# Kernel tuning notes

Measured on AMD Instinct MI355X. Metric: run time of the kernel, lower is better.

The kernel has to match this reference:

```python
import jax, jax.numpy as jnp
import numpy as np
from jax import lax

B, L, D, H = 2, 4096, 1024, 16
K = 4            # short conv kernel size
HD = D // H      # head dim = 64
EPS = 1e-5


def causal_dw_conv(x, w):
    # depthwise causal conv: x [B,L,D], w [D,K]
    xp = jnp.pad(x, ((0, 0), (K - 1, 0), (0, 0)))
    out = xp[:, 0:L, :] * w[:, 0]
    for j in range(1, K):
        out = out + xp[:, j:j + L, :] * w[:, j]
    return out


def setup_inputs() -> dict:
    key = jax.random.key(0)
    ks = jax.random.split(key, 10)
    s = 0.02
    return {
        "hidden_states": jax.random.normal(ks[0], (B, L, D), jnp.float32),
        "Wq": jax.random.normal(ks[1], (D, D), jnp.float32) * s,
        "Wk": jax.random.normal(ks[2], (D, D), jnp.float32) * s,
        "Wv": jax.random.normal(ks[3], (D, D), jnp.float32) * s,
        "Wb": jax.random.normal(ks[4], (D, H), jnp.float32) * s,
        "conv_q": jax.random.normal(ks[5], (D, K), jnp.float32) * s,
        "conv_k": jax.random.normal(ks[6], (D, K), jnp.float32) * s,
        "conv_v": jax.random.normal(ks[7], (D, K), jnp.float32) * s,
        "o_norm_w": jnp.ones((HD,), jnp.float32),
        "Wo": jax.random.normal(ks[8], (D, D), jnp.float32) * s,
    }


def reference(hidden_states, Wq, Wk, Wv, Wb, conv_q, conv_k, conv_v, o_norm_w, Wo):
    x = hidden_states
    # projections + short causal conv with SiLU (qk_activation == 'silu')
    q = jax.nn.silu(causal_dw_conv(x @ Wq, conv_q))
    k = jax.nn.silu(causal_dw_conv(x @ Wk, conv_k))
    v = jax.nn.silu(causal_dw_conv(x @ Wv, conv_v))

    # [B,L,D] -> [L,B,H,hd] for the time scan
    def to_heads(t):
        return t.reshape(B, L, H, HD).transpose(1, 0, 2, 3)

    q, k, v = to_heads(q), to_heads(k), to_heads(v)

    # l2 qk-norm
    q = q / jnp.linalg.norm(q, axis=-1, keepdims=True)
    k = k / jnp.linalg.norm(k, axis=-1, keepdims=True)

    # beta gate [L,B,H]
    beta = jax.nn.sigmoid(x @ Wb).transpose(1, 0, 2)

    def step(S, inp):
        qt, kt, vt, bt = inp  # [B,H,hd] x3, [B,H]
        v_old = jnp.einsum('bhk,bhkv->bhv', kt, S)
        delta = (vt - v_old) * bt[..., None]
        S = S + jnp.einsum('bhk,bhv->bhkv', kt, delta)
        ot = jnp.einsum('bhk,bhkv->bhv', qt, S)
        return S, ot

    S0 = jnp.zeros((B, H, HD, HD), x.dtype)
    _, o = lax.scan(step, S0, (q, k, v, beta))  # o: [L,B,H,hd]
    o = o.transpose(1, 0, 2, 3)  # [B,L,H,hd]

    # per-head RMSNorm
    rms = jax.lax.rsqrt(jnp.mean(o * o, axis=-1, keepdims=True) + EPS)
    o = o * rms * o_norm_w

    return o.reshape(B, L, D) @ Wo
```

## Files before the change

kernel.cpp:

```cpp
#include <hip/hip_runtime.h>
#include <hip/hip_bf16.h>
#include <math.h>

#define BB 2
#define LL 4096
#define DD 1024
#define HH 16
#define HDIM 64
#define CC 64
#define NC 64
#define BH 32
#define GG 8
#define GS 8

typedef __attribute__((ext_vector_type(8))) short short8;
typedef __attribute__((ext_vector_type(4))) float f32x4;
typedef unsigned short u16;

__device__ __forceinline__ u16 f2bf(float f) {
    unsigned int u = __float_as_uint(f);
    unsigned int r = (u + 0x7fffu + ((u >> 16) & 1u)) >> 16;
    return (u16)r;
}
__device__ __forceinline__ float bf2f(u16 h) {
    return __uint_as_float((unsigned)h << 16);
}
__device__ __forceinline__ void split2(float x, u16& h, u16& l) {
    h = f2bf(x);
    l = f2bf(x - bf2f(h));
}
__device__ __forceinline__ float4 ld_bf4(const u16* p) {
    uint2 v = *(const uint2*)p;
    return make_float4(bf2f((u16)v.x), bf2f((u16)(v.x >> 16)),
                       bf2f((u16)v.y), bf2f((u16)(v.y >> 16)));
}

__device__ __forceinline__ void gld_lds16(const void* g, void* l) {
    __builtin_amdgcn_global_load_lds(
        (const __attribute__((address_space(1))) void*)g,
        (__attribute__((address_space(3))) void*)l, 16, 0, 0);
}

__device__ __forceinline__ int swz(int r, int c) {
    return (r << 6) + ((((c >> 2) ^ (r >> 2)) & 15) << 2) + (c & 3);
}
__device__ __forceinline__ int swze(int r, int c) {
    return (r << 6) + (c ^ (((r ^ (r >> 3)) & 7) << 3));
}

__device__ __forceinline__ void mm64(const u16* __restrict__ Ah, const u16* __restrict__ Al,
                                     const u16* __restrict__ Bh, const u16* __restrict__ Bl,
                                     f32x4* acc, int w, int lane) {
    const int ln = lane & 15, kg = (lane >> 4) * 8;
#pragma unroll
    for (int kb = 0; kb < 2; ++kb) {
        const int k0 = kb * 32 + kg;
        short8 ah = *(const short8*)&Ah[swze(w * 16 + ln, k0)];
        short8 al = *(const short8*)&Al[swze(w * 16 + ln, k0)];
#pragma unroll
        for (int j = 0; j < 4; ++j) {
            short8 bh = *(const short8*)&Bh[swze(j * 16 + ln, k0)];
            short8 bl = *(const short8*)&Bl[swze(j * 16 + ln, k0)];
            acc[j] = __builtin_amdgcn_mfma_f32_16x16x32_bf16(ah, bh, acc[j], 0, 0, 0);
            acc[j] = __builtin_amdgcn_mfma_f32_16x16x32_bf16(ah, bl, acc[j], 0, 0, 0);
            acc[j] = __builtin_amdgcn_mfma_f32_16x16x32_bf16(al, bh, acc[j], 0, 0, 0);
        }
    }
}
__device__ __forceinline__ void mm64_bb(const u16* __restrict__ Ah,
                                        const u16* __restrict__ Bh,
                                        f32x4* acc, int w, int lane) {
    const int ln = lane & 15, kg = (lane >> 4) * 8;
#pragma unroll
    for (int kb = 0; kb < 2; ++kb) {
        const int k0 = kb * 32 + kg;
        short8 ah = *(const short8*)&Ah[swze(w * 16 + ln, k0)];
#pragma unroll
        for (int j = 0; j < 4; ++j) {
            short8 bh = *(const short8*)&Bh[swze(j * 16 + ln, k0)];
            acc[j] = __builtin_amdgcn_mfma_f32_16x16x32_bf16(ah, bh, acc[j], 0, 0, 0);
        }
    }
}
__device__ __forceinline__ void mm64_ab(const u16* __restrict__ Ah,
                                        const u16* __restrict__ Bh, const u16* __restrict__ Bl,
                                        f32x4* acc, int w, int lane) {
    const int ln = lane & 15, kg = (lane >> 4) * 8;
#pragma unroll
    for (int kb = 0; kb < 2; ++kb) {
        const int k0 = kb * 32 + kg;
        short8 ah = *(const short8*)&Ah[swze(w * 16 + ln, k0)];
#pragma unroll
        for (int j = 0; j < 4; ++j) {
            short8 bh = *(const short8*)&Bh[swze(j * 16 + ln, k0)];
            short8 bl = *(const short8*)&Bl[swze(j * 16 + ln, k0)];
            acc[j] = __builtin_amdgcn_mfma_f32_16x16x32_bf16(ah, bh, acc[j], 0, 0, 0);
            acc[j] = __builtin_amdgcn_mfma_f32_16x16x32_bf16(ah, bl, acc[j], 0, 0, 0);
        }
    }
}

__device__ __forceinline__ void g_to_ls(const float* __restrict__ G, u16* Ah, u16* Al, int tid) {
#pragma unroll
    for (int p = 0; p < 4; ++p) {
        int flat = p * 1024 + tid * 4;
        int r = flat >> 6, c = flat & 63;
        float4 v = *(const float4*)&G[flat];
        u16 h0, l0, h1, l1, h2, l2, h3, l3;
        split2(v.x, h0, l0); split2(v.y, h1, l1);
        split2(v.z, h2, l2); split2(v.w, h3, l3);
        int idx = swze(r, c);
        uint2 hv, lv;
        hv.x = (unsigned)h0 | ((unsigned)h1 << 16); hv.y = (unsigned)h2 | ((unsigned)h3 << 16);
        lv.x = (unsigned)l0 | ((unsigned)l1 << 16); lv.y = (unsigned)l2 | ((unsigned)l3 << 16);
        *(uint2*)&Ah[idx] = hv;
        *(uint2*)&Al[idx] = lv;
    }
}
__device__ __forceinline__ void g_to_ls_b(const u16* __restrict__ G16, u16* Ah, int tid) {
#pragma unroll
    for (int p = 0; p < 2; ++p) {
        int flat = p * 2048 + tid * 8;
        int r = flat >> 6, c = flat & 63;
        *(short8*)&Ah[swze(r, c)] = *(const short8*)&G16[flat];
    }
}

__device__ __forceinline__ void frag_to_ls(const f32x4* acc, u16* Ah, u16* Al, int w, int lane) {
    const int g = lane >> 4, ln = lane & 15;
#pragma unroll
    for (int j = 0; j < 4; ++j)
#pragma unroll
        for (int r = 0; r < 4; ++r) {
            int row = w * 16 + g * 4 + r, col = j * 16 + ln;
            u16 h, l; split2(acc[j][r], h, l);
            Ah[swze(row, col)] = h;
            Al[swze(row, col)] = l;
        }
}

__device__ __forceinline__ void g_to_frag(const float* __restrict__ G, f32x4* acc, int w, int lane) {
    const int g = lane >> 4, ln = lane & 15;
#pragma unroll
    for (int j = 0; j < 4; ++j)
#pragma unroll
        for (int r = 0; r < 4; ++r)
            acc[j][r] = G[(w * 16 + g * 4 + r) * 64 + j * 16 + ln];
}
__device__ __forceinline__ void g_add_frag(const float* __restrict__ G, f32x4* acc, int w, int lane) {
    const int g = lane >> 4, ln = lane & 15;
#pragma unroll
    for (int j = 0; j < 4; ++j)
#pragma unroll
        for (int r = 0; r < 4; ++r)
            acc[j][r] += G[(w * 16 + g * 4 + r) * 64 + j * 16 + ln];
}
__device__ __forceinline__ void frag_to_g(const f32x4* acc, float* __restrict__ G, int w, int lane) {
    const int g = lane >> 4, ln = lane & 15;
#pragma unroll
    for (int j = 0; j < 4; ++j)
#pragma unroll
        for (int r = 0; r < 4; ++r)
            G[(w * 16 + g * 4 + r) * 64 + j * 16 + ln] = acc[j][r];
}

__global__ __launch_bounds__(256) void cast_bf16_k(const float* __restrict__ in,
                                                   u16* __restrict__ out) {
    int i = (blockIdx.x * 256 + threadIdx.x) * 8;
    float4 a = *(const float4*)&in[i];
    float4 b = *(const float4*)&in[i + 4];
    uint4 o;
    o.x = (unsigned)f2bf(a.x) | ((unsigned)f2bf(a.y) << 16);
    o.y = (unsigned)f2bf(a.z) | ((unsigned)f2bf(a.w) << 16);
    o.z = (unsigned)f2bf(b.x) | ((unsigned)f2bf(b.y) << 16);
    o.w = (unsigned)f2bf(b.z) | ((unsigned)f2bf(b.w) << 16);
    *(uint4*)&out[i] = o;
}

__global__ __launch_bounds__(256) void transW4_k(const float* __restrict__ W0,
                                                 const float* __restrict__ W1,
                                                 const float* __restrict__ W2,
                                                 const float* __restrict__ W3,
                                                 u16* __restrict__ WT0) {
    __shared__ float t[32][33];
    const int which = blockIdx.z;
    const float* W = (which == 0) ? W0 : (which == 1) ? W1 : (which == 2) ? W2 : W3;
    u16* WT = WT0 + (size_t)which * 1048576;
    const int bx = blockIdx.x * 32, by = blockIdx.y * 32;
#pragma unroll
    for (int p = 0; p < 4; ++p) {
        int idx = p * 256 + threadIdx.x;
        int r = idx >> 5, cc = idx & 31;
        t[r][cc] = W[(size_t)(by + r) * 1024 + bx + cc];
    }
    __syncthreads();
#pragma unroll
    for (int p = 0; p < 4; ++p) {
        int idx = p * 256 + threadIdx.x;
        int r = idx >> 5, cc = idx & 31;
        WT[(size_t)(bx + r) * 1024 + by + cc] = f2bf(t[cc][r]);
    }
}

__device__ __forceinline__ void gemm_core(const u16* A, const u16* BT,
                                          int m0, int n0, f32x4 acc[4][4]) {
    __shared__ __align__(16) short As[2][128 * 32];
    __shared__ __align__(16) short Bs[2][128 * 32];
    const int tid = threadIdx.x;
    const int lane = tid & 63, w = tid >> 6;
    const int wr = w >> 1, wc = w & 1;
    const int ln15 = lane & 15;
    const int erow = tid >> 2;
    const int ecol = (((tid & 3) ^ ((erow >> 1) & 3)) << 3);
    const int kch = lane >> 4;

#define STAGE(buf, k0)                                                        \
    {                                                                         \
        _Pragma("unroll")                                                     \
        for (int r = 0; r < 2; ++r) {                                         \
            gld_lds16(A  + (size_t)(m0 + erow + r * 64) * 1024 + (k0) + ecol, \
                      (short*)As[buf] + r * 2048 + tid * 8);                  \
            gld_lds16(BT + (size_t)(n0 + erow + r * 64) * 1024 + (k0) + ecol, \
                      (short*)Bs[buf] + r * 2048 + tid * 8);                  \
        }                                                                     \
    }

#define COMPUTE(buf)                                                           \
    {                                                                          \
        short8 af[4], bf[4];                                                   \
        _Pragma("unroll")                                                      \
        for (int i = 0; i < 4; ++i) {                                          \
            int row = wr * 64 + i * 16 + ln15;                                 \
            af[i] = *(const short8*)&As[buf][row * 32 + ((kch ^ ((row >> 1) & 3)) << 3)]; \
        }                                                                      \
        _Pragma("unroll")                                                      \
        for (int j = 0; j < 4; ++j) {                                          \
            int row = wc * 64 + j * 16 + ln15;                                 \
            bf[j] = *(const short8*)&Bs[buf][row * 32 + ((kch ^ ((row >> 1) & 3)) << 3)]; \
        }                                                                      \
        __builtin_amdgcn_s_setprio(1);                                         \
        _Pragma("unroll")                                                      \
        for (int i = 0; i < 4; ++i)                                            \
            _Pragma("unroll")                                                  \
            for (int j = 0; j < 4; ++j)                                        \
                acc[i][j] = __builtin_amdgcn_mfma_f32_16x16x32_bf16(af[i], bf[j], acc[i][j], 0, 0, 0); \
        __builtin_amdgcn_s_setprio(0);                                         \
    }

    STAGE(0, 0);
    for (int t = 0; t < 31; ++t) {
        const int cur = t & 1;
        STAGE(cur ^ 1, (t + 1) * 32);
        asm volatile("s_waitcnt vmcnt(4)" ::: "memory");
        __builtin_amdgcn_sched_barrier(0);
        __builtin_amdgcn_s_barrier();
        COMPUTE(cur);
        asm volatile("s_waitcnt lgkmcnt(0)" ::: "memory");
        __builtin_amdgcn_sched_barrier(0);
        __builtin_amdgcn_s_barrier();
    }
    asm volatile("s_waitcnt vmcnt(0)" ::: "memory");
    __builtin_amdgcn_sched_barrier(0);
    __builtin_amdgcn_s_barrier();
    COMPUTE(1);
#undef STAGE
#undef COMPUTE
}

__global__ __launch_bounds__(256) void gemm_bf16(const u16* __restrict__ A,
                                                 const u16* __restrict__ BT,
                                                 float* __restrict__ C) {
    const int m0 = blockIdx.y * 128, n0 = blockIdx.x * 128;
    f32x4 acc[4][4] = {};
    gemm_core(A, BT, m0, n0, acc);
    const int lane = threadIdx.x & 63, w = threadIdx.x >> 6;
    const int crow0 = m0 + (w >> 1) * 64 + (lane >> 4) * 4;
    const int ccol0 = n0 + (w & 1) * 64 + (lane & 15);
#pragma unroll
    for (int i = 0; i < 4; ++i)
#pragma unroll
        for (int j = 0; j < 4; ++j)
#pragma unroll
            for (int r = 0; r < 4; ++r)
                C[(size_t)(crow0 + i * 16 + r) * 1024 + ccol0 + j * 16] = acc[i][j][r];
}

__global__ __launch_bounds__(256) void gemm_qkv(const u16* __restrict__ A,
                                                const u16* __restrict__ WT0,
                                                u16* __restrict__ xq16,
                                                u16* __restrict__ xk16,
                                                float* __restrict__ xv) {
    const int which = blockIdx.x >> 3;
    const int n0 = (blockIdx.x & 7) * 128;
    const int m0 = blockIdx.y * 128;
    const u16* BT = WT0 + (size_t)which * 1048576;
    f32x4 acc[4][4] = {};
    gemm_core(A, BT, m0, n0, acc);
    const int lane = threadIdx.x & 63, w = threadIdx.x >> 6;
    const int crow0 = m0 + (w >> 1) * 64 + (lane >> 4) * 4;
    const int ccol0 = n0 + (w & 1) * 64 + (lane & 15);
    if (which == 2) {
#pragma unroll
        for (int i = 0; i < 4; ++i)
#pragma unroll
            for (int j = 0; j < 4; ++j)
#pragma unroll
                for (int r = 0; r < 4; ++r)
                    xv[(size_t)(crow0 + i * 16 + r) * 1024 + ccol0 + j * 16] = acc[i][j][r];
    } else {
        u16* C16 = (which == 0) ? xq16 : xk16;
#pragma unroll
        for (int i = 0; i < 4; ++i)
#pragma unroll
            for (int j = 0; j < 4; ++j)
#pragma unroll
                for (int r = 0; r < 4; ++r)
                    C16[(size_t)(crow0 + i * 16 + r) * 1024 + ccol0 + j * 16] = f2bf(acc[i][j][r]);
    }
}

__global__ __launch_bounds__(256) void beta_k(const float* __restrict__ X,
                                              const float* __restrict__ Wb,
                                              float* __restrict__ beta) {
    int idx = blockIdx.x * 256 + threadIdx.x;
    int row = idx >> 4, h = idx & 15;
    const float* xr = X + (size_t)row * DD;
    float s = 0.f;
    for (int k4 = 0; k4 < DD; k4 += 4) {
        float4 xv = *(const float4*)&xr[k4];
        s += xv.x * Wb[(k4 + 0) * HH + h];
        s += xv.y * Wb[(k4 + 1) * HH + h];
        s += xv.z * Wb[(k4 + 2) * HH + h];
        s += xv.w * Wb[(k4 + 3) * HH + h];
    }
    float bv = 1.f / (1.f + expf(-s));
    int b = row >> 12, l = row & (LL - 1);
    beta[((size_t)b * HH + h) * LL + l] = bv;
}

__global__ __launch_bounds__(256) void conv3_k(const u16* __restrict__ xq16,
                                               const u16* __restrict__ xk16,
                                               const float* __restrict__ xv,
                                               const float* __restrict__ cwq,
                                               const float* __restrict__ cwk,
                                               const float* __restrict__ cwv,
                                               u16* __restrict__ q16,
                                               u16* __restrict__ k16,
                                               float* __restrict__ vout) {
    const int which = blockIdx.z;
    const float* cw = (which == 0) ? cwq : (which == 1) ? cwk : cwv;
    const int l0 = blockIdx.x * 16, b = blockIdx.y;
    const int tid = threadIdx.x;
    const int d0 = tid * 4;
    const float4 w0 = *(const float4*)&cw[(d0 + 0) * 4];
    const float4 w1 = *(const float4*)&cw[(d0 + 1) * 4];
    const float4 w2 = *(const float4*)&cw[(d0 + 2) * 4];
    const float4 w3 = *(const float4*)&cw[(d0 + 3) * 4];
    const int h = d0 >> 6, hd = d0 & 63;
    if (which < 2) {
        const u16* Xb = ((which == 0) ? xq16 : xk16) + (size_t)b * LL * DD;
        u16* O16 = (which == 0) ? q16 : k16;
        float4 xm3 = make_float4(0, 0, 0, 0), xm2 = xm3, xm1 = xm3;
        if (l0 > 0) {
            xm3 = ld_bf4(&Xb[(size_t)(l0 - 3) * DD + d0]);
            xm2 = ld_bf4(&Xb[(size_t)(l0 - 2) * DD + d0]);
            xm1 = ld_bf4(&Xb[(size_t)(l0 - 1) * DD + d0]);
        }
#pragma unroll
        for (int t = 0; t < 16; ++t) {
            const int l = l0 + t;
            float4 xc = ld_bf4(&Xb[(size_t)l * DD + d0]);
            float a0 = xm3.x * w0.x + xm2.x * w0.y + xm1.x * w0.z + xc.x * w0.w;
            float a1 = xm3.y * w1.x + xm2.y * w1.y + xm1.y * w1.z + xc.y * w1.w;
            float a2 = xm3.z * w2.x + xm2.z * w2.y + xm1.z * w2.z + xc.z * w2.w;
            float a3 = xm3.w * w3.x + xm2.w * w3.y + xm1.w * w3.z + xc.w * w3.w;
            a0 = a0 / (1.f + expf(-a0));
            a1 = a1 / (1.f + expf(-a1));
            a2 = a2 / (1.f + expf(-a2));
            a3 = a3 / (1.f + expf(-a3));
            float s = a0 * a0 + a1 * a1 + a2 * a2 + a3 * a3;
            s += __shfl_xor(s, 1);
            s += __shfl_xor(s, 2);
            s += __shfl_xor(s, 4);
            s += __shfl_xor(s, 8);
            float sc = rsqrtf(s);
            a0 *= sc; a1 *= sc; a2 *= sc; a3 *= sc;
            uint2 o;
            o.x = (unsigned)f2bf(a0) | ((unsigned)f2bf(a1) << 16);
            o.y = (unsigned)f2bf(a2) | ((unsigned)f2bf(a3) << 16);
            *(uint2*)&O16[(((size_t)b * HH + h) * LL + l) * 64 + hd] = o;
            xm3 = xm2; xm2 = xm1; xm1 = xc;
        }
    } else {
        const float* Xb = xv + (size_t)b * LL * DD;
        float4 xm3 = make_float4(0, 0, 0, 0), xm2 = xm3, xm1 = xm3;
        if (l0 > 0) {
            xm3 = *(const float4*)&Xb[(size_t)(l0 - 3) * DD + d0];
            xm2 = *(const float4*)&Xb[(size_t)(l0 - 2) * DD + d0];
            xm1 = *(const float4*)&Xb[(size_t)(l0 - 1) * DD + d0];
        }
#pragma unroll
        for (int t = 0; t < 16; ++t) {
            const int l = l0 + t;
            float4 xc = *(const float4*)&Xb[(size_t)l * DD + d0];
            float a0 = xm3.x * w0.x + xm2.x * w0.y + xm1.x * w0.z + xc.x * w0.w;
            float a1 = xm3.y * w1.x + xm2.y * w1.y + xm1.y * w1.z + xc.y * w1.w;
            float a2 = xm3.z * w2.x + xm2.z * w2.y + xm1.z * w2.z + xc.z * w2.w;
            float a3 = xm3.w * w3.x + xm2.w * w3.y + xm1.w * w3.z + xc.w * w3.w;
            a0 = a0 / (1.f + expf(-a0));
            a1 = a1 / (1.f + expf(-a1));
            a2 = a2 / (1.f + expf(-a2));
            a3 = a3 / (1.f + expf(-a3));
            *(float4*)&vout[(((size_t)b * HH + h) * LL + l) * 64 + hd] =
                make_float4(a0, a1, a2, a3);
            xm3 = xm2; xm2 = xm1; xm1 = xc;
        }
    }
}

__global__ __launch_bounds__(256) void phaseA5(const u16* __restrict__ kg16,
                                               const float* __restrict__ vg,
                                               const float* __restrict__ betag,
                                               float* __restrict__ Wg,
                                               float* __restrict__ UgT,
                                               float* __restrict__ Pall,
                                               float* __restrict__ BallT) {
    __shared__ __align__(16) char pool[73728];
    u16* Kh   = (u16*)pool;
    u16* KTh  = (u16*)(pool + 8192);
    float* At = (float*)(pool + 16384);
    float* WU = (float*)(pool + 32768);
    u16* WTh  = (u16*)pool;
    u16* WTl  = (u16*)(pool + 16384);
    u16* UTh  = (u16*)(pool + 24576);
    u16* UTl  = (u16*)(pool + 65536);
    float* scr = (float*)(pool + 32768);

    const int c = blockIdx.x, bh = blockIdx.y;
    const int tid = threadIdx.x, lane = tid & 63, w = tid >> 6;
    const int g = lane >> 4, ln = lane & 15;
    const int t0 = (tid >> 4) * 4, d4 = (tid & 15) * 4;
    const size_t base = ((size_t)bh * LL + (size_t)c * 64) * 64;
    const size_t obase = ((size_t)bh * NC + c) * 4096;
    const float* bet = betag + (size_t)bh * LL + (size_t)c * 64;

    g_to_ls_b(kg16 + base, Kh, tid);
    {
        u16 kv[4][4];
#pragma unroll
        for (int i = 0; i < 4; ++i) {
            uint2 v = *(const uint2*)&kg16[base + (size_t)(t0 + i) * 64 + d4];
            kv[i][0] = (u16)v.x; kv[i][1] = (u16)(v.x >> 16);
            kv[i][2] = (u16)v.y; kv[i][3] = (u16)(v.y >> 16);
        }
#pragma unroll
        for (int j = 0; j < 4; ++j) {
            uint2 hv;
            hv.x = (unsigned)kv[0][j] | ((unsigned)kv[1][j] << 16);
            hv.y = (unsigned)kv[2][j] | ((unsigned)kv[3][j] << 16);
            *(uint2*)&KTh[swze(d4 + j, t0)] = hv;
        }
    }
    __syncthreads();
    {
        f32x4 acc[4] = {};
        mm64_bb(Kh, Kh, acc, w, lane);
#pragma unroll
        for (int r = 0; r < 4; ++r) {
            int t = w * 16 + g * 4 + r;
            float bt = bet[t];
#pragma unroll
            for (int j = 0; j < 4; ++j) {
                int s = j * 16 + ln;
                At[t * 64 + s] = (s < t) ? bt * acc[j][r] : 0.f;
            }
        }
    }
#pragma unroll
    for (int p = 0; p < 8; ++p) {
        int flat = p * 1024 + tid * 4;
        int t = flat >> 7, j = flat & 127;
        float bt = bet[t];
        float4 src;
        if (j < 64) src = ld_bf4(&Kh[swze(t, j)]);
        else        src = *(const float4*)&vg[base + (size_t)t * 64 + (j - 64)];
        src.x *= bt; src.y *= bt; src.z *= bt; src.w *= bt;
        *(float4*)&WU[t * 128 + j] = src;
    }
    __syncthreads();
#pragma unroll
    for (int pb = 0; pb < 4; ++pb) {
        const int r0 = pb * 16;
        if (pb > 0) {
            const int col = tid & 127;
            const int rbase = r0 + (tid >> 7) * 8;
            float acc8[8] = {};
            for (int r = 0; r < r0; r += 4) {
                float u0 = WU[(r + 0) * 128 + col], u1 = WU[(r + 1) * 128 + col];
                float u2 = WU[(r + 2) * 128 + col], u3 = WU[(r + 3) * 128 + col];
#pragma unroll
                for (int i = 0; i < 8; ++i) {
                    float4 a4 = *(const float4*)&At[(rbase + i) * 64 + r];
                    acc8[i] += a4.x * u0 + a4.y * u1 + a4.z * u2 + a4.w * u3;
                }
            }
#pragma unroll
            for (int i = 0; i < 8; ++i) WU[(rbase + i) * 128 + col] -= acc8[i];
            __syncthreads();
        }
        if (tid < 128) {
            const int col = tid;
            float wv[16];
            wv[0] = WU[r0 * 128 + col];
#pragma unroll
            for (int t = 1; t < 16; ++t) {
                float a = WU[(r0 + t) * 128 + col];
#pragma unroll
                for (int r = 0; r < t; ++r) a -= At[(r0 + t) * 64 + r0 + r] * wv[r];
                wv[t] = a;
            }
#pragma unroll
            for (int t = 1; t < 16; ++t) WU[(r0 + t) * 128 + col] = wv[t];
        }
        __syncthreads();
    }
#pragma unroll
    for (int p = 0; p < 4; ++p) {
        int flat = p * 1024 + tid * 4;
        int t = flat >> 6, j = flat & 63;
        *(float4*)&Wg[obase + flat] = *(const float4*)&WU[t * 128 + j];
    }
    {
        u16 h4[4][4], l4[4][4];
#pragma unroll
        for (int i = 0; i < 4; ++i) {
            float4 v = *(const float4*)&WU[(t0 + i) * 128 + d4];
            split2(v.x, h4[i][0], l4[i][0]); split2(v.y, h4[i][1], l4[i][1]);
            split2(v.z, h4[i][2], l4[i][2]); split2(v.w, h4[i][3], l4[i][3]);
        }
#pragma unroll
        for (int j = 0; j < 4; ++j) {
            uint2 hv, lv;
            hv.x = (unsigned)h4[0][j] | ((unsigned)h4[1][j] << 16);
            hv.y = (unsigned)h4[2][j] | ((unsigned)h4[3][j] << 16);
            lv.x = (unsigned)l4[0][j] | ((unsigned)l4[1][j] << 16);
            lv.y = (unsigned)l4[2][j] | ((unsigned)l4[3][j] << 16);
            *(uint2*)&WTh[swze(d4 + j, t0)] = hv;
            *(uint2*)&WTl[swze(d4 + j, t0)] = lv;
        }
#pragma unroll
        for (int i = 0; i < 4; ++i) {
            float4 v = *(const float4*)&WU[(t0 + i) * 128 + 64 + d4];
            split2(v.x, h4[i][0], l4[i][0]); split2(v.y, h4[i][1], l4[i][1]);
            split2(v.z, h4[i][2], l4[i][2]); split2(v.w, h4[i][3], l4[i][3]);
        }
#pragma unroll
        for (int j = 0; j < 4; ++j) {
            uint2 hv, lv;
            hv.x = (unsigned)h4[0][j] | ((unsigned)h4[1][j] << 16);
            hv.y = (unsigned)h4[2][j] | ((unsigned)h4[3][j] << 16);
            lv.x = (unsigned)l4[0][j] | ((unsigned)l4[1][j] << 16);
            lv.y = (unsigned)l4[2][j] | ((unsigned)l4[3][j] << 16);
            *(uint2*)&UTh[swze(d4 + j, t0)] = hv;
            *(uint2*)&UTl[swze(d4 + j, t0)] = lv;
        }
    }
    __syncthreads();
#pragma unroll
    for (int p = 0; p < 4; ++p) {
        int flat = p * 1024 + tid * 4;
        int n = flat >> 6, tt = flat & 63;
        int idx = swze(n, tt);
        uint2 hh = *(const uint2*)&UTh[idx];
        uint2 ll2 = *(const uint2*)&UTl[idx];
        float4 o;
        o.x = bf2f((u16)hh.x) + bf2f((u16)ll2.x);
        o.y = bf2f((u16)(hh.x >> 16)) + bf2f((u16)(ll2.x >> 16));
        o.z = bf2f((u16)hh.y) + bf2f((u16)ll2.y);
        o.w = bf2f((u16)(hh.y >> 16)) + bf2f((u16)(ll2.y >> 16));
        *(float4*)&UgT[obase + flat] = o;
    }
    f32x4 aP[4] = {}, aB[4] = {};
    mm64_ab(KTh, WTh, WTl, aP, w, lane);
    mm64_ab(KTh, UTh, UTl, aB, w, lane);
#pragma unroll
    for (int j = 0; j < 4; ++j)
#pragma unroll
        for (int r = 0; r < 4; ++r) {
            int row = w * 16 + g * 4 + r, col = j * 16 + ln;
            float pv = ((row == col) ? 1.f : 0.f) - aP[j][r];
            Pall[obase + (size_t)row * 64 + col] = pv;
            scr[swz(row, col)] = aB[j][r];
        }
    __syncthreads();
#pragma unroll
    for (int p = 0; p < 4; ++p) {
        int flat = p * 1024 + tid * 4;
        int n = flat >> 6, dd = flat & 63;
        float4 o;
        o.x = scr[swz(dd + 0, n)];
        o.y = scr[swz(dd + 1, n)];
        o.z = scr[swz(dd + 2, n)];
        o.w = scr[swz(dd + 3, n)];
        *(float4*)&BallT[obase + flat] = o;
    }
}

__global__ __launch_bounds__(256) void compose3(const float* __restrict__ Pall,
                                                const float* __restrict__ BallT,
                                                float* __restrict__ Pg,
                                                float* __restrict__ BgT) {
    __shared__ __align__(16) char pool[81920];
    u16* Ph = (u16*)pool;
    u16* Pl = (u16*)(pool + 8192);
    u16* Bh = (u16*)(pool + 16384);
    u16* Bl = (u16*)(pool + 24576);
    u16* nh = (u16*)(pool + 32768);
    u16* nl = (u16*)(pool + 40960);
    float* scr = (float*)(pool + 49152);
    const int g = blockIdx.x, bh = blockIdx.y;
    const int tid = threadIdx.x, lane = tid & 63, w = tid >> 6;
    const int gi = lane >> 4, ln = lane & 15;
    const size_t base0 = ((size_t)bh * NC + (size_t)g * GS) * 4096;
    f32x4 mP[4], mB[4];
#pragma unroll
    for (int p = 0; p < 4; ++p) {
        int flat = p * 1024 + tid * 4;
        int r = flat >> 6, c4 = flat & 63;
        *(float4*)&scr[swz(r, c4)] = *(const float4*)&Pall[base0 + flat];
    }
    g_to_frag(BallT + base0, mB, w, lane);
    __syncthreads();
#pragma unroll
    for (int j = 0; j < 4; ++j)
#pragma unroll
        for (int r = 0; r < 4; ++r) {
            int row = w * 16 + gi * 4 + r, col = j * 16 + ln;
            mP[j][r] = scr[swz(col, row)];
        }
    for (int s = 1; s < GS; ++s) {
        __syncthreads();
        frag_to_ls(mP, Ph, Pl, w, lane);
        frag_to_ls(mB, Bh, Bl, w, lane);
        g_to_ls(&Pall[base0 + (size_t)s * 4096], nh, nl, tid);
        __syncthreads();
        f32x4 aP[4] = {}, aB[4] = {};
        mm64(Ph, Pl, nh, nl, aP, w, lane);
        mm64(Bh, Bl, nh, nl, aB, w, lane);
        g_add_frag(&BallT[base0 + (size_t)s * 4096], aB, w, lane);
#pragma unroll
        for (int j = 0; j < 4; ++j) { mP[j] = aP[j]; mB[j] = aB[j]; }
    }
    const size_t gbase = ((size_t)bh * GG + g) * 4096;
    frag_to_g(mB, BgT + gbase, w, lane);
    __syncthreads();
#pragma unroll
    for (int j = 0; j < 4; ++j)
#pragma unroll
        for (int r = 0; r < 4; ++r) {
            int row = w * 16 + gi * 4 + r, col = j * 16 + ln;
            scr[swz(row, col)] = mP[j][r];
        }
    __syncthreads();
#pragma unroll
    for (int p = 0; p < 4; ++p) {
        int flat = p * 1024 + tid * 4;
        int a = flat >> 6, b0 = flat & 63;
        float4 o;
        o.x = scr[swz(b0 + 0, a)];
        o.y = scr[swz(b0 + 1, a)];
        o.z = scr[swz(b0 + 2, a)];
        o.w = scr[swz(b0 + 3, a)];
        *(float4*)&Pg[gbase + flat] = o;
    }
}

__global__ __launch_bounds__(256) void scanG3(const float* __restrict__ Pg,
                                              const float* __restrict__ BgT,
                                              float* __restrict__ SallT) {
    __shared__ __align__(16) char pool[32768];
    u16* Sh = (u16*)pool;
    u16* Sl = (u16*)(pool + 8192);
    u16* nh = (u16*)(pool + 16384);
    u16* nl = (u16*)(pool + 24576);
    const int bh = blockIdx.x;
    const int tid = threadIdx.x, lane = tid & 63, w = tid >> 6;
    f32x4 mS[4] = {};
    for (int g = 0; g < GG; ++g) {
        const size_t sbase = ((size_t)bh * NC + (size_t)g * GS) * 4096;
        frag_to_g(mS, SallT + sbase, w, lane);
        if (g == GG - 1) break;
        __syncthreads();
        frag_to_ls(mS, Sh, Sl, w, lane);
        g_to_ls(&Pg[((size_t)bh * GG + g) * 4096], nh, nl, tid);
        __syncthreads();
        f32x4 a[4] = {};
        mm64(Sh, Sl, nh, nl, a, w, lane);
        g_add_frag(&BgT[((size_t)bh * GG + g) * 4096], a, w, lane);
#pragma unroll
        for (int j = 0; j < 4; ++j) mS[j] = a[j];
    }
}

__global__ __launch_bounds__(256) void rollout3(const float* __restrict__ Pall,
                                                const float* __restrict__ BallT,
                                                float* __restrict__ SallT) {
    __shared__ __align__(16) char pool[32768];
    u16* Sh = (u16*)pool;
    u16* Sl = (u16*)(pool + 8192);
    u16* nh = (u16*)(pool + 16384);
    u16* nl = (u16*)(pool + 24576);
    const int g = blockIdx.x, bh = blockIdx.y;
    const int tid = threadIdx.x, lane = tid & 63, w = tid >> 6;
    const size_t base0 = ((size_t)bh * NC + (size_t)g * GS) * 4096;
    f32x4 mS[4];
    g_to_frag(SallT + base0, mS, w, lane);
    for (int j = 1; j < GS; ++j) {
        __syncthreads();
        frag_to_ls(mS, Sh, Sl, w, lane);
        g_to_ls(&Pall[base0 + (size_t)(j - 1) * 4096], nh, nl, tid);
        __syncthreads();
        f32x4 a[4] = {};
        mm64(Sh, Sl, nh, nl, a, w, lane);
        g_add_frag(&BallT[base0 + (size_t)(j - 1) * 4096], a, w, lane);
#pragma unroll
        for (int jj = 0; jj < 4; ++jj) mS[jj] = a[jj];
        frag_to_g(mS, SallT + base0 + (size_t)j * 4096, w, lane);
    }
}

__global__ __launch_bounds__(256) void phaseO4(const float* __restrict__ Wg,
                                               const float* __restrict__ UgT,
                                               const u16* __restrict__ qg16,
                                               const u16* __restrict__ kg16,
                                               const float* __restrict__ SallT,
                                               const float* __restrict__ nw,
                                               u16* __restrict__ ob) {
    __shared__ __align__(16) char pool[57344];
    u16* Qh = (u16*)pool;
    u16* Kh = (u16*)(pool + 8192);
    u16* Wh = (u16*)(pool + 16384);
    u16* Wl = (u16*)(pool + 24576);
    u16* Sh = (u16*)(pool + 32768);
    u16* Sl = (u16*)(pool + 40960);
    u16* Dl = (u16*)(pool + 49152);
    u16* Dh = Kh;
    u16* Mh = Wh; u16* Ml = Wl;
    const int c = blockIdx.x, bh = blockIdx.y;
    const int b = bh >> 4, h = bh & 15;
    const int tid = threadIdx.x, lane = tid & 63, w = tid >> 6;
    const int gi = lane >> 4, ln = lane & 15;
    const size_t tbase = ((size_t)bh * NC + c) * 4096;
    const size_t qkbase = ((size_t)bh * LL + (size_t)c * 64) * 64;
    g_to_ls_b(qg16 + qkbase, Qh, tid);
    g_to_ls_b(kg16 + qkbase, Kh, tid);
    g_to_ls(&Wg[tbase], Wh, Wl, tid);
    g_to_ls(&SallT[tbase], Sh, Sl, tid);
    __syncthreads();
    f32x4 aM[4] = {}, aD[4] = {};
    mm64_bb(Qh, Kh, aM, w, lane);
    mm64(Sh, Sl, Wh, Wl, aD, w, lane);
    __syncthreads();
#pragma unroll
    for (int j = 0; j < 4; ++j)
#pragma unroll
        for (int r = 0; r < 4; ++r) {
            int row = w * 16 + gi * 4 + r, col = j * 16 + ln;
            float mv = (col <= row) ? aM[j][r] : 0.f;
            u16 mh_, ml_; split2(mv, mh_, ml_);
            Mh[swze(row, col)] = mh_;
            Ml[swze(row, col)] = ml_;
            float dv = UgT[tbase + (size_t)row * 64 + col] - aD[j][r];
            u16 dh_, dl_; split2(dv, dh_, dl_);
            Dh[swze(row, col)] = dh_;
            Dl[swze(row, col)] = dl_;
        }
    __syncthreads();
    f32x4 aO[4] = {};
    mm64_ab(Qh, Sh, Sl, aO, w, lane);
    mm64(Mh, Ml, Dh, Dl, aO, w, lane);
    float nwv[4];
#pragma unroll
    for (int j = 0; j < 4; ++j) nwv[j] = nw[j * 16 + ln];
#pragma unroll
    for (int r = 0; r < 4; ++r) {
        float ss = 0.f;
#pragma unroll
        for (int j = 0; j < 4; ++j) ss += aO[j][r] * aO[j][r];
        ss += __shfl_xor(ss, 1);
        ss += __shfl_xor(ss, 2);
        ss += __shfl_xor(ss, 4);
        ss += __shfl_xor(ss, 8);
        float rms = rsqrtf(ss * (1.f / 64.f) + 1e-5f);
        int row = w * 16 + gi * 4 + r;
        size_t orow = ((size_t)b * LL + (size_t)c * 64 + row) * DD + (size_t)h * 64;
#pragma unroll
        for (int j = 0; j < 4; ++j)
            ob[orow + j * 16 + ln] = f2bf(aO[j][r] * rms * nwv[j]);
    }
}

extern "C" void kernel_launch(void* const* d_in, const int* in_sizes, int n_in,
                              void* d_out, int out_size, void* d_ws, size_t ws_size,
                              hipStream_t stream) {
    const float* x  = (const float*)d_in[0];
    const float* Wq = (const float*)d_in[1];
    const float* Wk = (const float*)d_in[2];
    const float* Wv = (const float*)d_in[3];
    const float* Wb = (const float*)d_in[4];
    const float* cq = (const float*)d_in[5];
    const float* ck = (const float*)d_in[6];
    const float* cv = (const float*)d_in[7];
    const float* nw = (const float*)d_in[8];
    const float* Wo = (const float*)d_in[9];
    float* out = (float*)d_out;
    float* ws = (float*)d_ws;

    const size_t SZ = (size_t)BB * LL * DD;
    float* xv    = ws;
    float* v     = ws + SZ;
    float* Wg    = ws + 2 * SZ;
    float* UgT   = ws + 3 * SZ;
    float* SallT = ws + 4 * SZ;
    u16* xb   = (u16*)(ws + 5 * SZ);
    u16* q16  = xb;
    u16* xq16 = (u16*)(ws + 5 * SZ) + SZ;
    u16* xk16 = (u16*)(ws + 5 * SZ) + 2 * SZ;
    u16* k16  = (u16*)(ws + 5 * SZ) + 3 * SZ;
    float* beta = ws + 7 * SZ;
    u16* wqT  = (u16*)(beta + (size_t)BH * LL);
    float* PgB = (float*)(wqT + (size_t)4 * 1048576);
    float* BgT = PgB + 1048576;

    float* Pall  = xv;
    float* BallT = out;
    u16* ob   = (u16*)v;
    u16* woT  = wqT + (size_t)3 * 1048576;

    dim3 blk(256);

    cast_bf16_k<<<dim3(4096), blk, 0, stream>>>(x, xb);
    transW4_k<<<dim3(32, 32, 4), blk, 0, stream>>>(Wq, Wk, Wv, Wo, wqT);
    gemm_qkv<<<dim3(24, 64), blk, 0, stream>>>(xb, wqT, xq16, xk16, xv);
    beta_k<<<dim3(512), blk, 0, stream>>>(x, Wb, beta);
    conv3_k<<<dim3(LL / 16, BB, 3), blk, 0, stream>>>(xq16, xk16, xv, cq, ck, cv, q16, k16, v);
    phaseA5<<<dim3(NC, BH), blk, 0, stream>>>(k16, v, beta, Wg, UgT, Pall, BallT);
    compose3<<<dim3(GG, BH), blk, 0, stream>>>(Pall, BallT, PgB, BgT);
    scanG3<<<dim3(BH), blk, 0, stream>>>(PgB, BgT, SallT);
    rollout3<<<dim3(GG, BH), blk, 0, stream>>>(Pall, BallT, SallT);
    phaseO4<<<dim3(NC, BH), blk, 0, stream>>>(Wg, UgT, q16, k16, SallT, nw, ob);
    gemm_bf16<<<dim3(8, 64), blk, 0, stream>>>(ob, woT, out);
}
```

Measured before the change: 364.8 us.

## Store chunk intermediates as packed bf16 hi/lo pairs, prefetch, triple-buffer GEMM

Intermediate chunk matrices (W, U, P, B, S and the grouped P/B) are now written to global memory as packed 32-bit hi/lo bf16 pairs rather than fp32. Consumers can then load them straight into the split LDS tiles without calling split2 again. compose and rollout also prefetch the next chunk's P matrix into registers during the current matmul. Separately, the shared GEMM core goes from double to triple buffering with deeper vmcnt waits. In exchange it uses more LDS in the GEMM and more registers for the prefetch buffers.

```diff
diff --git a/kernel.cpp b/kernel.cpp
--- a/kernel.cpp
+++ b/kernel.cpp
@@ -16,6 +16,7 @@
 typedef __attribute__((ext_vector_type(8))) short short8;
 typedef __attribute__((ext_vector_type(4))) float f32x4;
 typedef unsigned short u16;
+typedef unsigned int u32;
 
 __device__ __forceinline__ u16 f2bf(float f) {
     unsigned int u = __float_as_uint(f);
@@ -28,6 +29,13 @@
 __device__ __forceinline__ void split2(float x, u16& h, u16& l) {
     h = f2bf(x);
     l = f2bf(x - bf2f(h));
+}
+__device__ __forceinline__ u32 packhl(float x) {
+    u16 h, l; split2(x, h, l);
+    return (u32)h | ((u32)l << 16);
+}
+__device__ __forceinline__ float unpackhl(u32 v) {
+    return bf2f((u16)v) + bf2f((u16)(v >> 16));
 }
 __device__ __forceinline__ float4 ld_bf4(const u16* p) {
     uint2 v = *(const uint2*)p;
@@ -126,6 +134,37 @@
     }
 }
 
+__device__ __forceinline__ void pload(uint4 pf[4], const u32* __restrict__ G, int tid) {
+    pf[0] = *(const uint4*)&G[tid * 8];
+    pf[1] = *(const uint4*)&G[tid * 8 + 4];
+    pf[2] = *(const uint4*)&G[2048 + tid * 8];
+    pf[3] = *(const uint4*)&G[2048 + tid * 8 + 4];
+}
+__device__ __forceinline__ void pstore_ls(const uint4 pf[4], u16* Ah, u16* Al, int tid) {
+#pragma unroll
+    for (int p = 0; p < 2; ++p) {
+        int flat = p * 2048 + tid * 8;
+        int r = flat >> 6, c = flat & 63;
+        uint4 a = pf[2 * p], b = pf[2 * p + 1];
+        short8 hi, lo;
+        hi[0] = (short)(u16)a.x; hi[1] = (short)(u16)a.y;
+        hi[2] = (short)(u16)a.z; hi[3] = (short)(u16)a.w;
+        hi[4] = (short)(u16)b.x; hi[5] = (short)(u16)b.y;
+        hi[6] = (short)(u16)b.z; hi[7] = (short)(u16)b.w;
+        lo[0] = (short)(a.x >> 16); lo[1] = (short)(a.y >> 16);
+        lo[2] = (short)(a.z >> 16); lo[3] = (short)(a.w >> 16);
+        lo[4] = (short)(b.x >> 16); lo[5] = (short)(b.y >> 16);
+        lo[6] = (short)(b.z >> 16); lo[7] = (short)(b.w >> 16);
+        *(short8*)&Ah[swze(r, c)] = hi;
+        *(short8*)&Al[swze(r, c)] = lo;
+    }
+}
+__device__ __forceinline__ void gp_to_ls(const u32* __restrict__ G, u16* Ah, u16* Al, int tid) {
+    uint4 pf[4];
+    pload(pf, G, tid);
+    pstore_ls(pf, Ah, Al, tid);
+}
+
 __device__ __forceinline__ void frag_to_ls(const f32x4* acc, u16* Ah, u16* Al, int w, int lane) {
     const int g = lane >> 4, ln = lane & 15;
 #pragma unroll
@@ -139,29 +178,29 @@
         }
 }
 
-__device__ __forceinline__ void g_to_frag(const float* __restrict__ G, f32x4* acc, int w, int lane) {
+__device__ __forceinline__ void gp_to_frag(const u32* __restrict__ G, f32x4* acc, int w, int lane) {
     const int g = lane >> 4, ln = lane & 15;
 #pragma unroll
     for (int j = 0; j < 4; ++j)
 #pragma unroll
         for (int r = 0; r < 4; ++r)
-            acc[j][r] = G[(w * 16 + g * 4 + r) * 64 + j * 16 + ln];
-}
-__device__ __forceinline__ void g_add_frag(const float* __restrict__ G, f32x4* acc, int w, int lane) {
+            acc[j][r] = unpackhl(G[(w * 16 + g * 4 + r) * 64 + j * 16 + ln]);
+}
+__device__ __forceinline__ void gp_add_frag(const u32* __restrict__ G, f32x4* acc, int w, int lane) {
     const int g = lane >> 4, ln = lane & 15;
 #pragma unroll
     for (int j = 0; j < 4; ++j)
 #pragma unroll
         for (int r = 0; r < 4; ++r)
-            acc[j][r] += G[(w * 16 + g * 4 + r) * 64 + j * 16 + ln];
-}
-__device__ __forceinline__ void frag_to_g(const f32x4* acc, float* __restrict__ G, int w, int lane) {
+            acc[j][r] += unpackhl(G[(w * 16 + g * 4 + r) * 64 + j * 16 + ln]);
+}
+__device__ __forceinline__ void frag_to_gp(const f32x4* acc, u32* __restrict__ G, int w, int lane) {
     const int g = lane >> 4, ln = lane & 15;
 #pragma unroll
     for (int j = 0; j < 4; ++j)
 #pragma unroll
         for (int r = 0; r < 4; ++r)
-            G[(w * 16 + g * 4 + r) * 64 + j * 16 + ln] = acc[j][r];
+            G[(w * 16 + g * 4 + r) * 64 + j * 16 + ln] = packhl(acc[j][r]);
 }
 
 __global__ __launch_bounds__(256) void cast_bf16_k(const float* __restrict__ in,
@@ -204,8 +243,8 @@
 
 __device__ __forceinline__ void gemm_core(const u16* A, const u16* BT,
                                           int m0, int n0, f32x4 acc[4][4]) {
-    __shared__ __align__(16) short As[2][128 * 32];
-    __shared__ __align__(16) short Bs[2][128 * 32];
+    __shared__ __align__(16) short As[3][128 * 32];
+    __shared__ __align__(16) short Bs[3][128 * 32];
     const int tid = threadIdx.x;
     const int lane = tid & 63, w = tid >> 6;
     const int wr = w >> 1, wc = w & 1;
@@ -248,17 +287,21 @@
     }
 
     STAGE(0, 0);
-    for (int t = 0; t < 31; ++t) {
-        const int cur = t & 1;
-        STAGE(cur ^ 1, (t + 1) * 32);
-        asm volatile("s_waitcnt vmcnt(4)" ::: "memory");
+    STAGE(1, 32);
+    for (int t = 0; t < 30; ++t) {
+        STAGE((t + 2) % 3, (t + 2) * 32);
+        asm volatile("s_waitcnt vmcnt(8)" ::: "memory");
         __builtin_amdgcn_sched_barrier(0);
         __builtin_amdgcn_s_barrier();
-        COMPUTE(cur);
+        COMPUTE(t % 3);
         asm volatile("s_waitcnt lgkmcnt(0)" ::: "memory");
         __builtin_amdgcn_sched_barrier(0);
         __builtin_amdgcn_s_barrier();
     }
+    asm volatile("s_waitcnt vmcnt(4)" ::: "memory");
+    __builtin_amdgcn_sched_barrier(0);
+    __builtin_amdgcn_s_barrier();
+    COMPUTE(0);
     asm volatile("s_waitcnt vmcnt(0)" ::: "memory");
     __builtin_amdgcn_sched_barrier(0);
     __builtin_amdgcn_s_barrier();
@@ -418,13 +461,13 @@
     }
 }
 
-__global__ __launch_bounds__(256) void phaseA5(const u16* __restrict__ kg16,
+__global__ __launch_bounds__(256) void phaseA6(const u16* __restrict__ kg16,
                                                const float* __restrict__ vg,
                                                const float* __restrict__ betag,
-                                               float* __restrict__ Wg,
-                                               float* __restrict__ UgT,
-                                               float* __restrict__ Pall,
-                                               float* __restrict__ BallT) {
+                                               u32* __restrict__ WgP,
+                                               u32* __restrict__ UgTP,
+                                               u32* __restrict__ PallP,
+                                               u32* __restrict__ BallTP) {
     __shared__ __align__(16) char pool[73728];
     u16* Kh   = (u16*)pool;
     u16* KTh  = (u16*)(pool + 8192);
@@ -528,7 +571,10 @@
     for (int p = 0; p < 4; ++p) {
         int flat = p * 1024 + tid * 4;
         int t = flat >> 6, j = flat & 63;
-        *(float4*)&Wg[obase + flat] = *(const float4*)&WU[t * 128 + j];
+        float4 v = *(const float4*)&WU[t * 128 + j];
+        uint4 o;
+        o.x = packhl(v.x); o.y = packhl(v.y); o.z = packhl(v.z); o.w = packhl(v.w);
+        *(uint4*)&WgP[obase + flat] = o;
     }
     {
         u16 h4[4][4], l4[4][4];
@@ -573,12 +619,12 @@
         int idx = swze(n, tt);
         uint2 hh = *(const uint2*)&UTh[idx];
         uint2 ll2 = *(const uint2*)&UTl[idx];
-        float4 o;
-        o.x = bf2f((u16)hh.x) + bf2f((u16)ll2.x);
-        o.y = bf2f((u16)(hh.x >> 16)) + bf2f((u16)(ll2.x >> 16));
-        o.z = bf2f((u16)hh.y) + bf2f((u16)ll2.y);
-        o.w = bf2f((u16)(hh.y >> 16)) + bf2f((u16)(ll2.y >> 16));
-        *(float4*)&UgT[obase + flat] = o;
+        uint4 o;
+        o.x = (hh.x & 0xffffu) | (ll2.x << 16);
+        o.y = (hh.x >> 16) | (ll2.x & 0xffff0000u);
+        o.z = (hh.y & 0xffffu) | (ll2.y << 16);
+        o.w = (hh.y >> 16) | (ll2.y & 0xffff0000u);
+        *(uint4*)&UgTP[obase + flat] = o;
     }
     f32x4 aP[4] = {}, aB[4] = {};
     mm64_ab(KTh, WTh, WTl, aP, w, lane);
@@ -589,7 +635,7 @@
         for (int r = 0; r < 4; ++r) {
             int row = w * 16 + g * 4 + r, col = j * 16 + ln;
             float pv = ((row == col) ? 1.f : 0.f) - aP[j][r];
-            Pall[obase + (size_t)row * 64 + col] = pv;
+            PallP[obase + (size_t)row * 64 + col] = packhl(pv);
             scr[swz(row, col)] = aB[j][r];
         }
     __syncthreads();
@@ -597,19 +643,19 @@
     for (int p = 0; p < 4; ++p) {
         int flat = p * 1024 + tid * 4;
         int n = flat >> 6, dd = flat & 63;
-        float4 o;
-        o.x = scr[swz(dd + 0, n)];
-        o.y = scr[swz(dd + 1, n)];
-        o.z = scr[swz(dd + 2, n)];
-        o.w = scr[swz(dd + 3, n)];
-        *(float4*)&BallT[obase + flat] = o;
-    }
-}
-
-__global__ __launch_bounds__(256) void compose3(const float* __restrict__ Pall,
-                                                const float* __restrict__ BallT,
-                                                float* __restrict__ Pg,
-                                                float* __restrict__ BgT) {
+        uint4 o;
+        o.x = packhl(scr[swz(dd + 0, n)]);
+        o.y = packhl(scr[swz(dd + 1, n)]);
+        o.z = packhl(scr[swz(dd + 2, n)]);
+        o.w = packhl(scr[swz(dd + 3, n)]);
+        *(uint4*)&BallTP[obase + flat] = o;
+    }
+}
+
+__global__ __launch_bounds__(256) void compose4(const u32* __restrict__ PallP,
+                                                const u32* __restrict__ BallTP,
+                                                u32* __restrict__ PgP,
+                                                u32* __restrict__ BgTP) {
     __shared__ __align__(16) char pool[81920];
     u16* Ph = (u16*)pool;
     u16* Pl = (u16*)(pool + 8192);
@@ -627,9 +673,11 @@
     for (int p = 0; p < 4; ++p) {
         int flat = p * 1024 + tid * 4;
         int r = flat >> 6, c4 = flat & 63;
-        *(float4*)&scr[swz(r, c4)] = *(const float4*)&Pall[base0 + flat];
-    }
-    g_to_frag(BallT + base0, mB, w, lane);
+        uint4 pk = *(const uint4*)&PallP[base0 + flat];
+        *(float4*)&scr[swz(r, c4)] =
+            make_float4(unpackhl(pk.x), unpackhl(pk.y), unpackhl(pk.z), unpackhl(pk.w));
+    }
+    gp_to_frag(BallTP + base0, mB, w, lane);
     __syncthreads();
 #pragma unroll
     for (int j = 0; j < 4; ++j)
@@ -638,21 +686,24 @@
             int row = w * 16 + gi * 4 + r, col = j * 16 + ln;
             mP[j][r] = scr[swz(col, row)];
         }
+    uint4 pf[4];
+    pload(pf, PallP + base0 + 4096, tid);
     for (int s = 1; s < GS; ++s) {
         __syncthreads();
         frag_to_ls(mP, Ph, Pl, w, lane);
         frag_to_ls(mB, Bh, Bl, w, lane);
-        g_to_ls(&Pall[base0 + (size_t)s * 4096], nh, nl, tid);
+        pstore_ls(pf, nh, nl, tid);
         __syncthreads();
+        if (s < GS - 1) pload(pf, PallP + base0 + (size_t)(s + 1) * 4096, tid);
         f32x4 aP[4] = {}, aB[4] = {};
         mm64(Ph, Pl, nh, nl, aP, w, lane);
         mm64(Bh, Bl, nh, nl, aB, w, lane);
-        g_add_frag(&BallT[base0 + (size_t)s * 4096], aB, w, lane);
+        gp_add_frag(BallTP + base0 + (size_t)s * 4096, aB, w, lane);
 #pragma unroll
         for (int j = 0; j < 4; ++j) { mP[j] = aP[j]; mB[j] = aB[j]; }
     }
     const size_t gbase = ((size_t)bh * GG + g) * 4096;
-    frag_to_g(mB, BgT + gbase, w, lane);
+    frag_to_gp(mB, BgTP + gbase, w, lane);
     __syncthreads();
 #pragma unroll
     for (int j = 0; j < 4; ++j)
@@ -666,18 +717,18 @@
     for (int p = 0; p < 4; ++p) {
         int flat = p * 1024 + tid * 4;
         int a = flat >> 6, b0 = flat & 63;
-        float4 o;
-        o.x = scr[swz(b0 + 0, a)];
-        o.y = scr[swz(b0 + 1, a)];
-        o.z = scr[swz(b0 + 2, a)];
-        o.w = scr[swz(b0 + 3, a)];
-        *(float4*)&Pg[gbase + flat] = o;
-    }
-}
-
-__global__ __launch_bounds__(256) void scanG3(const float* __restrict__ Pg,
-                                              const float* __restrict__ BgT,
-                                              float* __restrict__ SallT) {
+        uint4 o;
+        o.x = packhl(scr[swz(b0 + 0, a)]);
+        o.y = packhl(scr[swz(b0 + 1, a)]);
+        o.z = packhl(scr[swz(b0 + 2, a)]);
+        o.w = packhl(scr[swz(b0 + 3, a)]);
+        *(uint4*)&PgP[gbase + flat] = o;
+    }
+}
+
+__global__ __launch_bounds__(256) void scanG4(const u32* __restrict__ PgP,
+                                              const u32* __restrict__ BgTP,
+                                              u32* __restrict__ SallTP) {
     __shared__ __align__(16) char pool[32768];
     u16* Sh = (u16*)pool;
     u16* Sl = (u16*)(pool + 8192);
@@ -688,23 +739,23 @@
     f32x4 mS[4] = {};
     for (int g = 0; g < GG; ++g) {
         const size_t sbase = ((size_t)bh * NC + (size_t)g * GS) * 4096;
-        frag_to_g(mS, SallT + sbase, w, lane);
+        frag_to_gp(mS, SallTP + sbase, w, lane);
         if (g == GG - 1) break;
         __syncthreads();
         frag_to_ls(mS, Sh, Sl, w, lane);
-        g_to_ls(&Pg[((size_t)bh * GG + g) * 4096], nh, nl, tid);
+        gp_to_ls(PgP + ((size_t)bh * GG + g) * 4096, nh, nl, tid);
         __syncthreads();
         f32x4 a[4] = {};
         mm64(Sh, Sl, nh, nl, a, w, lane);
-        g_add_frag(&BgT[((size_t)bh * GG + g) * 4096], a, w, lane);
+        gp_add_frag(BgTP + ((size_t)bh * GG + g) * 4096, a, w, lane);
 #pragma unroll
         for (int j = 0; j < 4; ++j) mS[j] = a[j];
     }
 }
 
-__global__ __launch_bounds__(256) void rollout3(const float* __restrict__ Pall,
-                                                const float* __restrict__ BallT,
-                                                float* __restrict__ SallT) {
+__global__ __launch_bounds__(256) void rollout4(const u32* __restrict__ PallP,
+                                                const u32* __restrict__ BallTP,
+                                                u32* __restrict__ SallTP) {
     __shared__ __align__(16) char pool[32768];
     u16* Sh = (u16*)pool;
     u16* Sl = (u16*)(pool + 8192);
@@ -714,26 +765,29 @@
     const int tid = threadIdx.x, lane = tid & 63, w = tid >> 6;
     const size_t base0 = ((size_t)bh * NC + (size_t)g * GS) * 4096;
     f32x4 mS[4];
-    g_to_frag(SallT + base0, mS, w, lane);
+    gp_to_frag(SallTP + base0, mS, w, lane);
+    uint4 pf[4];
+    pload(pf, PallP + base0, tid);
     for (int j = 1; j < GS; ++j) {
         __syncthreads();
         frag_to_ls(mS, Sh, Sl, w, lane);
-        g_to_ls(&Pall[base0 + (size_t)(j - 1) * 4096], nh, nl, tid);
+        pstore_ls(pf, nh, nl, tid);
         __syncthreads();
+        if (j < GS - 1) pload(pf, PallP + base0 + (size_t)j * 4096, tid);
         f32x4 a[4] = {};
         mm64(Sh, Sl, nh, nl, a, w, lane);
-        g_add_frag(&BallT[base0 + (size_t)(j - 1) * 4096], a, w, lane);
+        gp_add_frag(BallTP + base0 + (size_t)(j - 1) * 4096, a, w, lane);
 #pragma unroll
         for (int jj = 0; jj < 4; ++jj) mS[jj] = a[jj];
-        frag_to_g(mS, SallT + base0 + (size_t)j * 4096, w, lane);
-    }
-}
-
-__global__ __launch_bounds__(256) void phaseO4(const float* __restrict__ Wg,
-                                               const float* __restrict__ UgT,
+        frag_to_gp(mS, SallTP + base0 + (size_t)j * 4096, w, lane);
+    }
+}
+
+__global__ __launch_bounds__(256) void phaseO5(const u32* __restrict__ WgP,
+                                               const u32* __restrict__ UgTP,
                                                const u16* __restrict__ qg16,
                                                const u16* __restrict__ kg16,
-                                               const float* __restrict__ SallT,
+                                               const u32* __restrict__ SallTP,
                                                const float* __restrict__ nw,
                                                u16* __restrict__ ob) {
     __shared__ __align__(16) char pool[57344];
@@ -754,8 +808,8 @@
     const size_t qkbase = ((size_t)bh * LL + (size_t)c * 64) * 64;
     g_to_ls_b(qg16 + qkbase, Qh, tid);
     g_to_ls_b(kg16 + qkbase, Kh, tid);
-    g_to_ls(&Wg[tbase], Wh, Wl, tid);
-    g_to_ls(&SallT[tbase], Sh, Sl, tid);
+    gp_to_ls(WgP + tbase, Wh, Wl, tid);
+    gp_to_ls(SallTP + tbase, Sh, Sl, tid);
     __syncthreads();
     f32x4 aM[4] = {}, aD[4] = {};
     mm64_bb(Qh, Kh, aM, w, lane);
@@ -770,7 +824,7 @@
             u16 mh_, ml_; split2(mv, mh_, ml_);
             Mh[swze(row, col)] = mh_;
             Ml[swze(row, col)] = ml_;
-            float dv = UgT[tbase + (size_t)row * 64 + col] - aD[j][r];
+            float dv = unpackhl(UgTP[tbase + (size_t)row * 64 + col]) - aD[j][r];
             u16 dh_, dl_; split2(dv, dh_, dl_);
             Dh[swze(row, col)] = dh_;
             Dl[swze(row, col)] = dl_;
@@ -819,9 +873,9 @@
     const size_t SZ = (size_t)BB * LL * DD;
     float* xv    = ws;
     float* v     = ws + SZ;
-    float* Wg    = ws + 2 * SZ;
-    float* UgT   = ws + 3 * SZ;
-    float* SallT = ws + 4 * SZ;
+    u32* WgP     = (u32*)(ws + 2 * SZ);
+    u32* UgTP    = (u32*)(ws + 3 * SZ);
+    u32* SallTP  = (u32*)(ws + 4 * SZ);
     u16* xb   = (u16*)(ws + 5 * SZ);
     u16* q16  = xb;
     u16* xq16 = (u16*)(ws + 5 * SZ) + SZ;
@@ -829,11 +883,11 @@
     u16* k16  = (u16*)(ws + 5 * SZ) + 3 * SZ;
     float* beta = ws + 7 * SZ;
     u16* wqT  = (u16*)(beta + (size_t)BH * LL);
-    float* PgB = (float*)(wqT + (size_t)4 * 1048576);
-    float* BgT = PgB + 1048576;
-
-    float* Pall  = xv;
-    float* BallT = out;
+    u32* PgP  = (u32*)(wqT + (size_t)4 * 1048576);
+    u32* BgTP = PgP + 1048576;
+
+    u32* PallP  = (u32*)xv;
+    u32* BallTP = (u32*)out;
     u16* ob   = (u16*)v;
     u16* woT  = wqT + (size_t)3 * 1048576;
 
@@ -844,10 +898,10 @@
     gemm_qkv<<<dim3(24, 64), blk, 0, stream>>>(xb, wqT, xq16, xk16, xv);
     beta_k<<<dim3(512), blk, 0, stream>>>(x, Wb, beta);
     conv3_k<<<dim3(LL / 16, BB, 3), blk, 0, stream>>>(xq16, xk16, xv, cq, ck, cv, q16, k16, v);
-    phaseA5<<<dim3(NC, BH), blk, 0, stream>>>(k16, v, beta, Wg, UgT, Pall, BallT);
-    compose3<<<dim3(GG, BH), blk, 0, stream>>>(Pall, BallT, PgB, BgT);
-    scanG3<<<dim3(BH), blk, 0, stream>>>(PgB, BgT, SallT);
-    rollout3<<<dim3(GG, BH), blk, 0, stream>>>(Pall, BallT, SallT);
-    phaseO4<<<dim3(NC, BH), blk, 0, stream>>>(Wg, UgT, q16, k16, SallT, nw, ob);
+    phaseA6<<<dim3(NC, BH), blk, 0, stream>>>(k16, v, beta, WgP, UgTP, PallP, BallTP);
+    compose4<<<dim3(GG, BH), blk, 0, stream>>>(PallP, BallTP, PgP, BgTP);
+    scanG4<<<dim3(BH), blk, 0, stream>>>(PgP, BgTP, SallTP);
+    rollout4<<<dim3(GG, BH), blk, 0, stream>>>(PallP, BallTP, SallTP);
+    phaseO5<<<dim3(NC, BH), blk, 0, stream>>>(WgP, UgTP, q16, k16, SallTP, nw, ob);
     gemm_bf16<<<dim3(8, 64), blk, 0, stream>>>(ob, woT, out);
 }
```

Result: no change. 362.9 us (-0.5%).
